# Kernel optimization log

Measured on AMD Instinct MI355X. Metric: run time of the kernel, lower is better.

## Reference

```python
import jax, jax.numpy as jnp
import numpy as np
import itertools


def _identity_grid(n, d, h, w, dtype):
    # Replicates AffineGridGenerator with identity theta:
    # linspace(-1,1,K) per axis (align_corners=True convention),
    # grid[..., 0]=x(W), grid[...,1]=y(H), grid[...,2]=z(D).
    zs = jnp.linspace(-1.0, 1.0, d, dtype=dtype) if d > 1 else jnp.array([-1.0], dtype=dtype)
    ys = jnp.linspace(-1.0, 1.0, h, dtype=dtype) if h > 1 else jnp.array([-1.0], dtype=dtype)
    xs = jnp.linspace(-1.0, 1.0, w, dtype=dtype) if w > 1 else jnp.array([-1.0], dtype=dtype)
    gz, gy, gx = jnp.meshgrid(zs, ys, xs, indexing='ij')  # [D,H,W]
    grid = jnp.stack([gx, gy, gz], axis=-1)               # [D,H,W,3]
    return jnp.broadcast_to(grid, (n, d, h, w, 3))


def _trilinear_sample(x, grid):
    N, C, Din, Hin, Win = x.shape
    dt = x.dtype
    fx = (grid[..., 0] + 1.0) * 0.5 * (Win - 1)
    fy = (grid[..., 1] + 1.0) * 0.5 * (Hin - 1)
    fz = (grid[..., 2] + 1.0) * 0.5 * (Din - 1)
    x0 = jnp.floor(fx); y0 = jnp.floor(fy); z0 = jnp.floor(fz)
    wx1 = (fx - x0).astype(dt); wy1 = (fy - y0).astype(dt); wz1 = (fz - z0).astype(dt)
    wx = (1.0 - wx1, wx1); wy = (1.0 - wy1, wy1); wz = (1.0 - wz1, wz1)
    ix = (x0.astype(jnp.int32), x0.astype(jnp.int32) + 1)
    iy = (y0.astype(jnp.int32), y0.astype(jnp.int32) + 1)
    iz = (z0.astype(jnp.int32), z0.astype(jnp.int32) + 1)

    def gather(xb, izb, iyb, ixb):
        return xb[:, izb, iyb, ixb]  # [C,D,H,W]
    gather_b = jax.vmap(gather)

    out = jnp.zeros((N, C) + grid.shape[1:4], dtype=dt)
    for a, b, c in itertools.product((0, 1), repeat=3):  # (z,y,x) corner
        zi, yi, xi = iz[a], iy[b], ix[c]
        valid = ((zi >= 0) & (zi < Din) & (yi >= 0) & (yi < Hin)
                 & (xi >= 0) & (xi < Win))
        zi = jnp.clip(zi, 0, Din - 1)
        yi = jnp.clip(yi, 0, Hin - 1)
        xi = jnp.clip(xi, 0, Win - 1)
        wgt = (wz[a] * wy[b] * wx[c]) * valid.astype(dt)  # [N,D,H,W]
        vals = gather_b(x, zi, yi, xi)                     # [N,C,D,H,W]
        out = out + vals * wgt[:, None]
    return out


def reference(x, d_out, h_out, w_out, variance):
    if variance:
        x = jnp.exp(x / 2.0)
    grid = _identity_grid(x.shape[0], d_out, h_out, w_out, x.dtype)
    out = _trilinear_sample(x, grid)
    if variance:
        out = jnp.log(out) * 2.0
    return out


def setup_inputs() -> dict:
    key = jax.random.key(0)
    x = jax.random.normal(key, (8, 32, 32, 64, 64), dtype=jnp.float32)
    return {"x": x, "d_out": 48, "h_out": 96, "w_out": 96, "variance": 1}
```

## Files before the change

kernel.cpp:

```cpp
#include <hip/hip_runtime.h>

constexpr int N = 8, C = 32, Din = 32, Hin = 64, Win = 64;
constexpr int Do = 48, Ho = 96, Wo = 96;

constexpr int BLOCK   = 256;
constexpr int NBLOCKS = N * C * Do;
constexpr int HROWS   = Ho / 2;
constexpr int F2PAD   = 68;
constexpr int QUADS   = HROWS * (Wo / 4);

__global__ __launch_bounds__(BLOCK)
void resample3d_var_kernel(const float* __restrict__ in, float* __restrict__ out) {
    __shared__ float G[Hin][Win];
    __shared__ float F2[HROWS][F2PAD];

    const int tid = threadIdx.x;
    const int bid = blockIdx.x;
    const int zo  = bid % Do;
    const int nc  = bid / Do;

    float fz  = (float)(zo * (Din - 1)) * (1.0f / (float)(Do - 1));
    int   z0  = (int)fz;
    float wz1 = fz - (float)z0;
    int   z1  = min(z0 + 1, Din - 1);
    float wz0 = 1.0f - wz1;

    const float* __restrict__ p0 = in + ((size_t)nc * Din + z0) * (Hin * Win);
    const float* __restrict__ p1 = in + ((size_t)nc * Din + z1) * (Hin * Win);

    {
        const int sy = tid >> 4;
        const int sx = (tid & 15) << 2;
#pragma unroll
        for (int k = 0; k < 4; ++k) {
            int y = sy + k * 16;
            const float4 a = *reinterpret_cast<const float4*>(p0 + y * Win + sx);
            const float4 b = *reinterpret_cast<const float4*>(p1 + y * Win + sx);
            float4 g;
            g.x = wz0 * __expf(a.x * 0.5f) + wz1 * __expf(b.x * 0.5f);
            g.y = wz0 * __expf(a.y * 0.5f) + wz1 * __expf(b.y * 0.5f);
            g.z = wz0 * __expf(a.z * 0.5f) + wz1 * __expf(b.z * 0.5f);
            g.w = wz0 * __expf(a.w * 0.5f) + wz1 * __expf(b.w * 0.5f);
            *reinterpret_cast<float4*>(&G[y][sx]) = g;
        }
    }
    __syncthreads();

    const size_t obase = ((size_t)nc * Do + zo) * (size_t)(Ho * Wo);
    constexpr float TWO_LN2 = 1.3862943611198906f;

    for (int h = 0; h < 2; ++h) {
        {
            const int x   = tid & 63;
            const int yr0 = tid >> 6;
#pragma unroll
            for (int j = 0; j < 12; ++j) {
                int yrow = j * 4 + yr0;
                int yo   = h * HROWS + yrow;
                float fy  = (float)(yo * (Hin - 1)) * (1.0f / (float)(Ho - 1));
                int   y0  = (int)fy;
                float wy1 = fy - (float)y0;
                int   y1  = min(y0 + 1, Hin - 1);
                float g0 = G[y0][x], g1 = G[y1][x];
                F2[yrow][x] = g0 + wy1 * (g1 - g0);
            }
        }
        __syncthreads();

        float* __restrict__ ob = out + obase + (size_t)h * (HROWS * Wo);
#pragma unroll
        for (int k = 0; k < 5; ++k) {
            int c = k * BLOCK + tid;
            if (c < QUADS) {
                int row = (c * 2731) >> 16;
                int q   = c - row * 24;
                float4 o;
                float* op = &o.x;
#pragma unroll
                for (int i = 0; i < 4; ++i) {
                    int   xo  = q * 4 + i;
                    float fx  = (float)(xo * (Win - 1)) * (1.0f / (float)(Wo - 1));
                    int   x0  = (int)fx;
                    float wx1 = fx - (float)x0;
                    int   x1  = min(x0 + 1, Win - 1);
                    float F0 = F2[row][x0], F1 = F2[row][x1];
                    float v  = F0 + wx1 * (F1 - F0);
                    op[i] = TWO_LN2 * __log2f(v);
                }
                *reinterpret_cast<float4*>(ob + (size_t)c * 4) = o;
            }
        }
        if (h == 0) __syncthreads();
    }
}

extern "C" void kernel_launch(void* const* d_in, const int* in_sizes, int n_in,
                              void* d_out, int out_size, void* d_ws, size_t ws_size,
                              hipStream_t stream) {
    const float* x = (const float*)d_in[0];
    float* out = (float*)d_out;
    resample3d_var_kernel<<<NBLOCKS, BLOCK, 0, stream>>>(x, out);
}
```

Measured before the change: 124.9 us.

## Fuse H and W interpolation into one pass with nontemporal stores

Drops the intermediate F2 shared buffer and its two extra barriers. Each output quad now reads four G values per point and does the bilinear H/W interpolation in registers. The exp is written as a raw exp2 builtin with a prescaled constant, the G rows are padded, and output uses nontemporal vector stores. This trades more LDS reads per output (4 instead of 2) for fewer barriers and less shared memory.

```diff
diff --git a/kernel.cpp b/kernel.cpp
--- a/kernel.cpp
+++ b/kernel.cpp
@@ -5,14 +5,13 @@
 
 constexpr int BLOCK   = 256;
 constexpr int NBLOCKS = N * C * Do;
-constexpr int HROWS   = Ho / 2;
-constexpr int F2PAD   = 68;
-constexpr int QUADS   = HROWS * (Wo / 4);
+constexpr int GPAD    = 68;
+
+typedef float f32x4 __attribute__((ext_vector_type(4)));
 
 __global__ __launch_bounds__(BLOCK)
 void resample3d_var_kernel(const float* __restrict__ in, float* __restrict__ out) {
-    __shared__ float G[Hin][Win];
-    __shared__ float F2[HROWS][F2PAD];
+    __shared__ float G[Hin][GPAD];
 
     const int tid = threadIdx.x;
     const int bid = blockIdx.x;
@@ -28,6 +27,8 @@
     const float* __restrict__ p0 = in + ((size_t)nc * Din + z0) * (Hin * Win);
     const float* __restrict__ p1 = in + ((size_t)nc * Din + z1) * (Hin * Win);
 
+    constexpr float HALF_LOG2E = 0.7213475204444817f;
+
     {
         const int sy = tid >> 4;
         const int sx = (tid & 15) << 2;
@@ -37,60 +38,47 @@
             const float4 a = *reinterpret_cast<const float4*>(p0 + y * Win + sx);
             const float4 b = *reinterpret_cast<const float4*>(p1 + y * Win + sx);
             float4 g;
-            g.x = wz0 * __expf(a.x * 0.5f) + wz1 * __expf(b.x * 0.5f);
-            g.y = wz0 * __expf(a.y * 0.5f) + wz1 * __expf(b.y * 0.5f);
-            g.z = wz0 * __expf(a.z * 0.5f) + wz1 * __expf(b.z * 0.5f);
-            g.w = wz0 * __expf(a.w * 0.5f) + wz1 * __expf(b.w * 0.5f);
+            g.x = wz0 * __builtin_amdgcn_exp2f(a.x * HALF_LOG2E) + wz1 * __builtin_amdgcn_exp2f(b.x * HALF_LOG2E);
+            g.y = wz0 * __builtin_amdgcn_exp2f(a.y * HALF_LOG2E) + wz1 * __builtin_amdgcn_exp2f(b.y * HALF_LOG2E);
+            g.z = wz0 * __builtin_amdgcn_exp2f(a.z * HALF_LOG2E) + wz1 * __builtin_amdgcn_exp2f(b.z * HALF_LOG2E);
+            g.w = wz0 * __builtin_amdgcn_exp2f(a.w * HALF_LOG2E) + wz1 * __builtin_amdgcn_exp2f(b.w * HALF_LOG2E);
             *reinterpret_cast<float4*>(&G[y][sx]) = g;
         }
     }
     __syncthreads();
 
-    const size_t obase = ((size_t)nc * Do + zo) * (size_t)(Ho * Wo);
+    float* __restrict__ ob = out + ((size_t)nc * Do + zo) * (size_t)(Ho * Wo);
     constexpr float TWO_LN2 = 1.3862943611198906f;
 
-    for (int h = 0; h < 2; ++h) {
-        {
-            const int x   = tid & 63;
-            const int yr0 = tid >> 6;
+#pragma unroll 3
+    for (int k = 0; k < 9; ++k) {
+        int c   = k * BLOCK + tid;
+        int row = (c * 2731) >> 16;
+        int q   = c - row * 24;
+
+        float fy  = (float)(row * (Hin - 1)) * (1.0f / (float)(Ho - 1));
+        int   y0  = (int)fy;
+        float wy1 = fy - (float)y0;
+        int   y1  = min(y0 + 1, Hin - 1);
+        const float* __restrict__ g0 = &G[y0][0];
+        const float* __restrict__ g1 = &G[y1][0];
+
+        f32x4 o;
 #pragma unroll
-            for (int j = 0; j < 12; ++j) {
-                int yrow = j * 4 + yr0;
-                int yo   = h * HROWS + yrow;
-                float fy  = (float)(yo * (Hin - 1)) * (1.0f / (float)(Ho - 1));
-                int   y0  = (int)fy;
-                float wy1 = fy - (float)y0;
-                int   y1  = min(y0 + 1, Hin - 1);
-                float g0 = G[y0][x], g1 = G[y1][x];
-                F2[yrow][x] = g0 + wy1 * (g1 - g0);
-            }
+        for (int i = 0; i < 4; ++i) {
+            int   xo  = q * 4 + i;
+            float fx  = (float)(xo * (Win - 1)) * (1.0f / (float)(Wo - 1));
+            int   x0  = (int)fx;
+            float wx1 = fx - (float)x0;
+            int   x1  = min(x0 + 1, Win - 1);
+            float a0 = g0[x0], a1 = g0[x1];
+            float b0 = g1[x0], b1 = g1[x1];
+            float fa = a0 + wy1 * (b0 - a0);
+            float fb = a1 + wy1 * (b1 - a1);
+            float v  = fa + wx1 * (fb - fa);
+            o[i] = TWO_LN2 * __log2f(v);
         }
-        __syncthreads();
-
-        float* __restrict__ ob = out + obase + (size_t)h * (HROWS * Wo);
-#pragma unroll
-        for (int k = 0; k < 5; ++k) {
-            int c = k * BLOCK + tid;
-            if (c < QUADS) {
-                int row = (c * 2731) >> 16;
-                int q   = c - row * 24;
-                float4 o;
-                float* op = &o.x;
-#pragma unroll
-                for (int i = 0; i < 4; ++i) {
-                    int   xo  = q * 4 + i;
-                    float fx  = (float)(xo * (Win - 1)) * (1.0f / (float)(Wo - 1));
-                    int   x0  = (int)fx;
-                    float wx1 = fx - (float)x0;
-                    int   x1  = min(x0 + 1, Win - 1);
-                    float F0 = F2[row][x0], F1 = F2[row][x1];
-                    float v  = F0 + wx1 * (F1 - F0);
-                    op[i] = TWO_LN2 * __log2f(v);
-                }
-                *reinterpret_cast<float4*>(ob + (size_t)c * 4) = o;
-            }
-        }
-        if (h == 0) __syncthreads();
+        __builtin_nontemporal_store(o, reinterpret_cast<f32x4*>(ob + (size_t)c * 4));
     }
 }
 
```

Result: slower. 137.1 us (+9.8%).

## Split each output slice into two H-halves per block with swizzled block order

Applied to the files above, without the earlier changes.

Each block now handles one half of the output H rows for a given (n,c,zo). It loads only the 33 input rows that half needs and does a single F2 pass, which doubles the block count and shrinks shared memory. Block IDs are remapped with an XCD-style swizzle, and launch bounds now request 7 waves per EU. The exp is computed with a raw exp2 builtin using a folded constant. The cost is about 3% redundant input loads and exp work on the shared boundary row, plus more block launches.

```diff
diff --git a/kernel.cpp b/kernel.cpp
--- a/kernel.cpp
+++ b/kernel.cpp
@@ -4,20 +4,30 @@
 constexpr int Do = 48, Ho = 96, Wo = 96;
 
 constexpr int BLOCK   = 256;
-constexpr int NBLOCKS = N * C * Do;
-constexpr int HROWS   = Ho / 2;
+constexpr int NBLOCKS = N * C * Do * 2;
+constexpr int GROWS   = 33;
+constexpr int GCHUNKS = GROWS * (Win / 4);
+constexpr int HROWS   = 48;
 constexpr int F2PAD   = 68;
 constexpr int QUADS   = HROWS * (Wo / 4);
 
-__global__ __launch_bounds__(BLOCK)
+typedef float f32x4 __attribute__((ext_vector_type(4)));
+
+__global__ __launch_bounds__(BLOCK, 7)
 void resample3d_var_kernel(const float* __restrict__ in, float* __restrict__ out) {
-    __shared__ float G[Hin][Win];
+    __shared__ float G[GROWS][Win];
     __shared__ float F2[HROWS][F2PAD];
 
     const int tid = threadIdx.x;
+
     const int bid = blockIdx.x;
-    const int zo  = bid % Do;
-    const int nc  = bid / Do;
+    const int sid = (bid & 7) * (NBLOCKS / 8) + (bid >> 3);
+
+    const int yhalf = sid & 1;
+    const int pz    = sid >> 1;
+    const int zo    = pz % Do;
+    const int nc    = pz / Do;
+    const int ybase = yhalf ? 31 : 0;
 
     float fz  = (float)(zo * (Din - 1)) * (1.0f / (float)(Do - 1));
     int   z0  = (int)fz;
@@ -25,72 +35,67 @@
     int   z1  = min(z0 + 1, Din - 1);
     float wz0 = 1.0f - wz1;
 
-    const float* __restrict__ p0 = in + ((size_t)nc * Din + z0) * (Hin * Win);
-    const float* __restrict__ p1 = in + ((size_t)nc * Din + z1) * (Hin * Win);
+    const float* __restrict__ p0 = in + ((size_t)nc * Din + z0) * (Hin * Win) + ybase * Win;
+    const float* __restrict__ p1 = in + ((size_t)nc * Din + z1) * (Hin * Win) + ybase * Win;
 
-    {
-        const int sy = tid >> 4;
-        const int sx = (tid & 15) << 2;
+    constexpr float HALF_LOG2E = 0.7213475204444817f;
+    constexpr float TWO_LN2    = 1.3862943611198906f;
+
 #pragma unroll
-        for (int k = 0; k < 4; ++k) {
-            int y = sy + k * 16;
+    for (int k = 0; k < 3; ++k) {
+        int c = k * BLOCK + tid;
+        if (c < GCHUNKS) {
+            int y  = c >> 4;
+            int sx = (c & 15) << 2;
             const float4 a = *reinterpret_cast<const float4*>(p0 + y * Win + sx);
             const float4 b = *reinterpret_cast<const float4*>(p1 + y * Win + sx);
             float4 g;
-            g.x = wz0 * __expf(a.x * 0.5f) + wz1 * __expf(b.x * 0.5f);
-            g.y = wz0 * __expf(a.y * 0.5f) + wz1 * __expf(b.y * 0.5f);
-            g.z = wz0 * __expf(a.z * 0.5f) + wz1 * __expf(b.z * 0.5f);
-            g.w = wz0 * __expf(a.w * 0.5f) + wz1 * __expf(b.w * 0.5f);
+            g.x = wz0 * __builtin_amdgcn_exp2f(a.x * HALF_LOG2E) + wz1 * __builtin_amdgcn_exp2f(b.x * HALF_LOG2E);
+            g.y = wz0 * __builtin_amdgcn_exp2f(a.y * HALF_LOG2E) + wz1 * __builtin_amdgcn_exp2f(b.y * HALF_LOG2E);
+            g.z = wz0 * __builtin_amdgcn_exp2f(a.z * HALF_LOG2E) + wz1 * __builtin_amdgcn_exp2f(b.z * HALF_LOG2E);
+            g.w = wz0 * __builtin_amdgcn_exp2f(a.w * HALF_LOG2E) + wz1 * __builtin_amdgcn_exp2f(b.w * HALF_LOG2E);
             *reinterpret_cast<float4*>(&G[y][sx]) = g;
         }
     }
     __syncthreads();
 
-    const size_t obase = ((size_t)nc * Do + zo) * (size_t)(Ho * Wo);
-    constexpr float TWO_LN2 = 1.3862943611198906f;
+    {
+        const int x = tid & 63;
+        const int w = tid >> 6;
+#pragma unroll
+        for (int j = 0; j < 12; ++j) {
+            int   yrow = j * 4 + w;
+            int   yo   = yhalf * HROWS + yrow;
+            float fy   = (float)(yo * (Hin - 1)) * (1.0f / (float)(Ho - 1));
+            int   y0   = (int)fy;
+            float wy1  = fy - (float)y0;
+            int   y1   = min(y0 + 1, Hin - 1);
+            float g0 = G[y0 - ybase][x], g1 = G[y1 - ybase][x];
+            F2[yrow][x] = g0 + wy1 * (g1 - g0);
+        }
+    }
+    __syncthreads();
 
-    for (int h = 0; h < 2; ++h) {
-        {
-            const int x   = tid & 63;
-            const int yr0 = tid >> 6;
+    float* __restrict__ ob = out + (((size_t)nc * Do + zo) * Ho + yhalf * HROWS) * Wo;
 #pragma unroll
-            for (int j = 0; j < 12; ++j) {
-                int yrow = j * 4 + yr0;
-                int yo   = h * HROWS + yrow;
-                float fy  = (float)(yo * (Hin - 1)) * (1.0f / (float)(Ho - 1));
-                int   y0  = (int)fy;
-                float wy1 = fy - (float)y0;
-                int   y1  = min(y0 + 1, Hin - 1);
-                float g0 = G[y0][x], g1 = G[y1][x];
-                F2[yrow][x] = g0 + wy1 * (g1 - g0);
+    for (int k = 0; k < 5; ++k) {
+        int c = k * BLOCK + tid;
+        if (c < QUADS) {
+            int row = (c * 2731) >> 16;
+            int q   = c - row * 24;
+            f32x4 o;
+#pragma unroll
+            for (int i = 0; i < 4; ++i) {
+                int   xo  = q * 4 + i;
+                float fx  = (float)(xo * (Win - 1)) * (1.0f / (float)(Wo - 1));
+                int   x0  = (int)fx;
+                float wx1 = fx - (float)x0;
+                int   x1  = min(x0 + 1, Win - 1);
+                float F0 = F2[row][x0], F1 = F2[row][x1];
+                o[i] = TWO_LN2 * __log2f(F0 + wx1 * (F1 - F0));
             }
+            *reinterpret_cast<f32x4*>(ob + (size_t)c * 4) = o;
         }
-        __syncthreads();
-
-        float* __restrict__ ob = out + obase + (size_t)h * (HROWS * Wo);
-#pragma unroll
-        for (int k = 0; k < 5; ++k) {
-            int c = k * BLOCK + tid;
-            if (c < QUADS) {
-                int row = (c * 2731) >> 16;
-                int q   = c - row * 24;
-                float4 o;
-                float* op = &o.x;
-#pragma unroll
-                for (int i = 0; i < 4; ++i) {
-                    int   xo  = q * 4 + i;
-                    float fx  = (float)(xo * (Win - 1)) * (1.0f / (float)(Wo - 1));
-                    int   x0  = (int)fx;
-                    float wx1 = fx - (float)x0;
-                    int   x1  = min(x0 + 1, Win - 1);
-                    float F0 = F2[row][x0], F1 = F2[row][x1];
-                    float v  = F0 + wx1 * (F1 - F0);
-                    op[i] = TWO_LN2 * __log2f(v);
-                }
-                *reinterpret_cast<float4*>(ob + (size_t)c * 4) = o;
-            }
-        }
-        if (h == 0) __syncthreads();
     }
 }
 
```

New measurement: 139.7 us. +11.8%, slower.
